# Kernel optimization log

Measured on AMD Instinct MI355X. Metric: run time of the kernel, lower is better.

The kernel has to match this reference:

```python
import jax, jax.numpy as jnp
import numpy as np
from jax import lax

# HATS hyperparameters (match torch module defaults)
H, W = 180, 240          # input frame (already a multiple of k -> no padding)
K = 10                   # cell size
R = 3                    # neighborhood radius
TAU = 1e6                # exponential decay constant (us)
DELTA_T = 1e5            # temporal window (us)
GH, GW = H // K, W // K
NC = GH * GW             # 432 cells
S = 2 * R + 1            # 7x7 local surface


def setup_inputs() -> dict:
    key = jax.random.key(0)
    k1, k2, k3, k4, k5 = jax.random.split(key, 5)
    B, T = 8, 2048
    x = jax.random.randint(k1, (B, T), 0, W)
    y = jax.random.randint(k2, (B, T), 0, H)
    # timestamps sorted per sequence (events arrive in temporal order)
    t = jnp.sort(jax.random.uniform(k3, (B, T), minval=0.0, maxval=3e5), axis=1)
    p = jax.random.randint(k4, (B, T), 0, 2)
    events = jnp.stack([x.astype(jnp.float32), y.astype(jnp.float32), t,
                        p.astype(jnp.float32)], axis=-1)  # [B, T, 4] = (x, y, t, p)
    lengths = jax.random.randint(k5, (B,), T // 2, T + 1)  # valid prefix length per sample
    return {"events": events, "lengths": lengths}


def reference(events, lengths):
    """HATS forward (bins=1, fold=False): returns [B, NCells, 2, 2R+1, 2R+1].

    Equivalent math to grouping events into per-cell memories, computing the
    exponentially-decayed local time surface of every event over its causal
    same-cell, same-polarity, delta_t-window neighbors, summing the surfaces
    per cell and dividing by the cell event count. Expressed here as a masked
    pairwise computation + segment scatter, which preserves the irregular
    scatter/gather structure without dynamic shapes.
    """
    B, T, _ = events.shape
    t = events[..., 2]
    x = lax.stop_gradient(events[..., 0]).astype(jnp.int32)
    y = lax.stop_gradient(events[..., 1]).astype(jnp.int32)
    p = lax.stop_gradient(events[..., 3]).astype(jnp.int32)

    valid = jnp.arange(T)[None, :] < lengths[:, None]          # [B, T]
    cell = (y // K) * GW + (x // K)                            # coord2cellid lookup, [B, T]

    # pair [b, i, j]: i = center event, j = (causal) contributing event
    dt = t[:, :, None] - t[:, None, :]                         # t_i - t_j, [B, T, T]
    dx = x[:, None, :] - x[:, :, None] + R                     # x_j - x_i + R
    dy = y[:, None, :] - y[:, :, None] + R                     # y_j - y_i + R
    ij = jnp.arange(T)
    causal = ij[None, :, None] >= ij[None, None, :]            # j <= i (incl. self)
    mask = (valid[:, :, None] & valid[:, None, :] & causal
            & (cell[:, :, None] == cell[:, None, :])
            & (p[:, :, None] == p[:, None, :])
            & (dt >= 0.0) & (dt <= DELTA_T)
            & (dx >= 0) & (dx < S) & (dy >= 0) & (dy < S))
    contrib = jnp.where(mask, jnp.exp(-dt / TAU), 0.0)

    # scatter-add each pair contribution into hist[b, cell_i, p_i, dy, dx]
    b_idx = jnp.arange(B)[:, None, None]
    seg = (((b_idx * NC + cell[:, :, None]) * 2 + p[:, :, None]) * S + dy) * S + dx
    seg = jnp.where(mask, seg, 0)
    hist = jax.ops.segment_sum(contrib.ravel(), seg.ravel(),
                               num_segments=B * NC * 2 * S * S)
    hist = hist.reshape(B, NC, 2, S, S)

    # normalize by number of events in each cell (clamped to >= 1)
    cseg = jnp.arange(B)[:, None] * NC + cell
    counts = jax.ops.segment_sum(jnp.where(valid, 1.0, 0.0).ravel(), cseg.ravel(),
                                 num_segments=B * NC)
    counts = jnp.maximum(counts, 1.0).reshape(B, NC, 1, 1, 1)
    return hist / counts
```

## Files before the change

kernel.cpp:

```cpp
#include <hip/hip_runtime.h>

#define KK 10
#define RR 3
#define TAU_F 1.0e6f
#define DELTA_T_F 1.0e5f
#define GW_ 24
#define NC_ 432
#define SS_ 7
#define NBIN 98
#define MAXEV 2048

__global__ __launch_bounds__(256) void hats_cell_kernel(
        const float4* __restrict__ ev,
        const int* __restrict__ lengths,
        float* __restrict__ out,
        int T) {
    __shared__ int   s_idx[MAXEV];
    __shared__ float s_hist[NBIN];
    __shared__ int   s_n;

    int blk  = blockIdx.x;
    int b    = blk / NC_;
    int cell = blk - b * NC_;
    int tid  = threadIdx.x;

    if (tid == 0) s_n = 0;
    if (tid < NBIN) s_hist[tid] = 0.0f;
    __syncthreads();

    int len = lengths[b];
    const float4* evb = ev + (size_t)b * T;

    for (int j = tid; j < len; j += 256) {
        float4 e = evb[j];
        int cj = ((int)e.y / KK) * GW_ + ((int)e.x / KK);
        if (cj == cell) {
            int slot = atomicAdd(&s_n, 1);
            s_idx[slot] = j;
        }
    }
    __syncthreads();

    int n = s_n;

    for (int pidx = tid; pidx < n * n; pidx += 256) {
        int ai = pidx / n;
        int aj = pidx - ai * n;
        int ii = s_idx[ai];
        int jj = s_idx[aj];
        if (jj > ii) continue;
        float4 e_i = evb[ii];
        float4 e_j = evb[jj];
        if ((int)e_j.w != (int)e_i.w) continue;
        float dt = e_i.z - e_j.z;
        if (dt > DELTA_T_F) continue;
        int dx = (int)e_j.x - (int)e_i.x + RR;
        int dy = (int)e_j.y - (int)e_i.y + RR;
        if ((unsigned)dx >= SS_ || (unsigned)dy >= SS_) continue;
        int p = (int)e_i.w;
        atomicAdd(&s_hist[(p * SS_ + dy) * SS_ + dx],
                  __expf(-dt * (1.0f / TAU_F)));
    }
    __syncthreads();

    float inv = __frcp_rn(fmaxf((float)n, 1.0f));
    float* obase = out + (size_t)blk * NBIN;
    if (tid < NBIN) obase[tid] = s_hist[tid] * inv;
}

extern "C" void kernel_launch(void* const* d_in, const int* in_sizes, int n_in,
                              void* d_out, int out_size, void* d_ws, size_t ws_size,
                              hipStream_t stream) {
    const float* events = (const float*)d_in[0];
    const int* lengths  = (const int*)d_in[1];
    float* out = (float*)d_out;

    int B = in_sizes[1];
    int T = in_sizes[0] / (B * 4);

    hats_cell_kernel<<<B * NC_, 256, 0, stream>>>(
        (const float4*)events, lengths, out, T);
}
```

Measured before the change: 61.28 us.

## Process groups of six cells per block with packed shared-memory event keys

Each block now handles six adjacent cells instead of one, so every event array is scanned by six times fewer blocks. Matching events are packed into shared-memory keys (x, y, polarity, local cell, index) plus timestamps, so the pair loop reads from shared memory instead of global memory. The cost is a larger pair space per block, since pairs across different cells in the group are tested and rejected, plus a hard assumption that T is at most 2048.

```diff
diff --git a/kernel.cpp b/kernel.cpp
--- a/kernel.cpp
+++ b/kernel.cpp
@@ -8,64 +8,91 @@
 #define NC_ 432
 #define SS_ 7
 #define NBIN 98
+#define G_ 6
+#define NGRP (NC_ / G_)
 #define MAXEV 2048
 
-__global__ __launch_bounds__(256) void hats_cell_kernel(
+__global__ __launch_bounds__(256) void hats_group_kernel(
         const float4* __restrict__ ev,
         const int* __restrict__ lengths,
         float* __restrict__ out,
         int T) {
-    __shared__ int   s_idx[MAXEV];
-    __shared__ float s_hist[NBIN];
-    __shared__ int   s_n;
+    __shared__ float s_t[MAXEV];
+    __shared__ int   s_key[MAXEV];
+    __shared__ float s_hist[G_ * NBIN];
+    __shared__ float s_inv[G_];
+    __shared__ int   s_cnt[G_];
+    __shared__ int   s_m;
 
-    int blk  = blockIdx.x;
-    int b    = blk / NC_;
-    int cell = blk - b * NC_;
-    int tid  = threadIdx.x;
+    int blk = blockIdx.x;
+    int b   = blk / NGRP;
+    int g   = blk - b * NGRP;
+    int c0  = g * G_;
+    int tid = threadIdx.x;
 
-    if (tid == 0) s_n = 0;
-    if (tid < NBIN) s_hist[tid] = 0.0f;
+    if (tid == 0) s_m = 0;
+    if (tid < G_) s_cnt[tid] = 0;
+    for (int o = tid; o < G_ * NBIN; o += 256) s_hist[o] = 0.0f;
     __syncthreads();
 
     int len = lengths[b];
     const float4* evb = ev + (size_t)b * T;
 
-    for (int j = tid; j < len; j += 256) {
-        float4 e = evb[j];
-        int cj = ((int)e.y / KK) * GW_ + ((int)e.x / KK);
-        if (cj == cell) {
-            int slot = atomicAdd(&s_n, 1);
-            s_idx[slot] = j;
+    float4 e[8];
+#pragma unroll
+    for (int k = 0; k < 8; ++k) {
+        int j = tid + (k << 8);
+        int ja = j < len ? j : (len - 1);
+        e[k] = evb[ja];
+    }
+#pragma unroll
+    for (int k = 0; k < 8; ++k) {
+        int j = tid + (k << 8);
+        if (j < len) {
+            int xi = (int)e[k].x;
+            int yi = (int)e[k].y;
+            int cell = (yi / KK) * GW_ + (xi / KK);
+            int local = cell - c0;
+            if ((unsigned)local < G_) {
+                int slot = atomicAdd(&s_m, 1);
+                s_t[slot] = e[k].z;
+                s_key[slot] = xi | (yi << 8) | ((int)e[k].w << 16)
+                            | (local << 17) | (j << 20);
+                atomicAdd(&s_cnt[local], 1);
+            }
         }
     }
     __syncthreads();
 
-    int n = s_n;
+    int m = s_m;
 
-    for (int pidx = tid; pidx < n * n; pidx += 256) {
-        int ai = pidx / n;
-        int aj = pidx - ai * n;
-        int ii = s_idx[ai];
-        int jj = s_idx[aj];
-        if (jj > ii) continue;
-        float4 e_i = evb[ii];
-        float4 e_j = evb[jj];
-        if ((int)e_j.w != (int)e_i.w) continue;
-        float dt = e_i.z - e_j.z;
+    for (int pidx = tid; pidx < m * m; pidx += 256) {
+        int ia = pidx / m;
+        int ib = pidx - ia * m;
+        int ka = s_key[ia];
+        int kb = s_key[ib];
+        if ((kb >> 20) > (ka >> 20)) continue;
+        if (((ka ^ kb) & 0x000F0000) != 0) continue;
+        float dt = s_t[ia] - s_t[ib];
         if (dt > DELTA_T_F) continue;
-        int dx = (int)e_j.x - (int)e_i.x + RR;
-        int dy = (int)e_j.y - (int)e_i.y + RR;
+        int dx = (kb & 0xFF) - (ka & 0xFF) + RR;
+        int dy = ((kb >> 8) & 0xFF) - ((ka >> 8) & 0xFF) + RR;
         if ((unsigned)dx >= SS_ || (unsigned)dy >= SS_) continue;
-        int p = (int)e_i.w;
-        atomicAdd(&s_hist[(p * SS_ + dy) * SS_ + dx],
+        int local = (ka >> 17) & 7;
+        int p     = (ka >> 16) & 1;
+        atomicAdd(&s_hist[local * NBIN + (p * SS_ + dy) * SS_ + dx],
                   __expf(-dt * (1.0f / TAU_F)));
     }
     __syncthreads();
 
-    float inv = __frcp_rn(fmaxf((float)n, 1.0f));
-    float* obase = out + (size_t)blk * NBIN;
-    if (tid < NBIN) obase[tid] = s_hist[tid] * inv;
+    if (tid < G_) s_inv[tid] = __frcp_rn(fmaxf((float)s_cnt[tid], 1.0f));
+    __syncthreads();
+
+    float* obase = out + ((size_t)(b * NC_ + c0)) * NBIN;
+    for (int o = tid; o < G_ * NBIN; o += 256) {
+        int c = o / NBIN;
+        obase[o] = s_hist[o] * s_inv[c];
+    }
 }
 
 extern "C" void kernel_launch(void* const* d_in, const int* in_sizes, int n_in,
@@ -78,6 +105,6 @@
     int B = in_sizes[1];
     int T = in_sizes[0] / (B * 4);
 
-    hats_cell_kernel<<<B * NC_, 256, 0, stream>>>(
+    hats_group_kernel<<<B * NGRP, 256, 0, stream>>>(
         (const float4*)events, lengths, out, T);
 }
```

After: 59.21 us. -3.4%, faster.
